# Kernel tuning notes

Hardware: AMD Instinct MI355X
Metric: run time of the kernel (lower is better)

The kernel has to match this reference:

```python
import jax, jax.numpy as jnp
import numpy as np

EMB = 384
HID = 256
HEADS = 4
HD = HID // HEADS  # 64
LAYERS = 2
M_DOCS = 32
TOTAL = 4096  # 1 query + 32 docs + 4063 sentences
LN_EPS = 1e-5


def _layernorm(x, scale, bias):
    mu = jnp.mean(x, axis=-1, keepdims=True)
    var = jnp.mean(jnp.square(x - mu), axis=-1, keepdims=True)
    return (x - mu) * jax.lax.rsqrt(var + LN_EPS) * scale + bias


def setup_inputs() -> dict:
    key = jax.random.key(0)
    ks = jax.random.split(key, 12)
    g = 0.05  # small init scale (stand-in for xavier)
    return {
        "node_embeddings": jax.random.normal(ks[0], (TOTAL, EMB), jnp.float32),
        "adj": jax.random.randint(ks[1], (TOTAL, TOTAL), 0, 2, jnp.int32),
        "num_docs": M_DOCS,
        "proj_w": jax.random.normal(ks[2], (HID, EMB), jnp.float32) * g,
        "proj_b": jnp.zeros((HID,), jnp.float32),
        "ln_scale": jnp.ones((LAYERS, HID), jnp.float32),
        "ln_bias": jnp.zeros((LAYERS, HID), jnp.float32),
        "gat_W": jax.random.normal(ks[3], (LAYERS, HEADS, HD, HID), jnp.float32) * g,
        "gat_a": jax.random.normal(ks[4], (LAYERS, HEADS, 2 * HD), jnp.float32) * g,
        "fusion_w": jax.random.normal(ks[5], (HID, 2 * HID + 2), jnp.float32) * g,
        "fusion_b": jnp.zeros((HID,), jnp.float32),
        "out_w": jax.random.normal(ks[6], (HID,), jnp.float32) * g,
        "out_b": jnp.float32(0.5),
    }


def reference(node_embeddings, adj, num_docs, proj_w, proj_b, ln_scale, ln_bias,
              gat_W, gat_a, fusion_w, fusion_b, out_w, out_b):
    T = node_embeddings.shape[0]
    M = num_docs
    N = T - 1 - M  # number of sentences
    # input projection + relu (dropout = identity in eval)
    h = jax.nn.relu(node_embeddings @ proj_w.T + proj_b)  # (T, HID)
    # query-guided sentence re-weighting
    q = h[0:1]                     # (1, HID)
    s = h[1 + M:]                  # (N, HID)
    qn = q / (jnp.linalg.norm(q, axis=1, keepdims=True) + 1e-8)
    sn = s / (jnp.linalg.norm(s, axis=1, keepdims=True) + 1e-8)
    cos = (qn @ sn.T).reshape(-1, 1)          # (N,1)
    s = s + 0.8 * q * cos
    h = jnp.concatenate([h[:1 + M], s], axis=0)
    mask = (adj == 0)[None]                   # (1,T,T)
    for i in range(LAYERS):
        res = h
        x = _layernorm(h, ln_scale[i], ln_bias[i])
        Wh = jnp.einsum('nd,hkd->hnk', x, gat_W[i])                # (H,T,HD)
        # concat-attention a.[Wh_i ; Wh_j] == a_src.Wh_i + a_dst.Wh_j
        src = jnp.einsum('hnk,hk->hn', Wh, gat_a[i, :, :HD])       # (H,T)
        dst = jnp.einsum('hnk,hk->hn', Wh, gat_a[i, :, HD:])       # (H,T)
        e = jax.nn.leaky_relu(src[:, :, None] + dst[:, None, :], 0.2)  # (H,T,T)
        e = jnp.where(mask, -jnp.inf, e)
        attn = jax.nn.softmax(e, axis=-1)                          # softmax over j
        hn = jnp.einsum('hij,hjk->hik', attn, Wh)                  # (H,T,HD)
        hcat = jnp.transpose(hn, (1, 0, 2)).reshape(T, HEADS * HD)
        h = 0.5 * jax.nn.relu(hcat) + 0.5 * res
    qh = h[0:1]
    sh = h[1 + M:]
    scores = (qh @ sh.T) / (HID ** 0.5)       # (1,N)
    aw = jax.nn.softmax(scores, axis=-1)
    awT = aw.T                                # (N,1)
    qw = qh * (awT + 0.5)                     # (N,HID)
    qnf = qh / (jnp.linalg.norm(qh, axis=1, keepdims=True) + 1e-8)
    snf = sh / (jnp.linalg.norm(sh, axis=1, keepdims=True) + 1e-8)
    cosf = (qnf @ snf.T).reshape(-1, 1)       # (N,1)
    feat = jnp.concatenate([sh, qw, cosf, awT], axis=1)  # (N, 2*HID+2)
    g = jax.nn.relu(feat @ fusion_w.T + fusion_b)
    out = g @ out_w + out_b                   # (N,)
    return out + 0.5 * cosf[:, 0]
```

## Files before the change

### kernel.cpp

```cpp
#include <hip/hip_runtime.h>
#include <hip/hip_bf16.h>
#include <stdint.h>

#define TOTAL 4096
#define EMB 384
#define MD 32
#define NDOCS (TOTAL - 1 - MD)
#define LN_EPS 1e-5f

typedef __hip_bfloat16 bf16;
typedef unsigned short ushort_t;
typedef __attribute__((ext_vector_type(8))) short short8;
typedef __attribute__((ext_vector_type(4))) float f32x4;
typedef __attribute__((ext_vector_type(2))) float f32x2;

__device__ __forceinline__ float ldf(const void* p, int i, int isbf) {
    return isbf ? __bfloat162float(((const bf16*)p)[i]) : ((const float*)p)[i];
}

__device__ __forceinline__ unsigned f2bf(float x) {
    return (__float_as_uint(x) + 0x8000u) >> 16;
}

__device__ __forceinline__ unsigned fenc(float f) {
    unsigned u = __float_as_uint(f);
    return (u >> 31) ? ~u : (u | 0x80000000u);
}
__device__ __forceinline__ float fdec(unsigned k) {
    return __uint_as_float((k & 0x80000000u) ? (k & 0x7FFFFFFFu) : ~k);
}

#define NTRANS ((EMB * 256 + 2 * 65536 + 514 * 256) / 256)
__global__ void k_adjmask(const int* adj, unsigned long long* maskb,
                          const uint16_t* embp, int* flag, unsigned* dmaxu,
                          const void* proj_w, const void* gat_W, const void* fusion_w,
                          float* projT, float* gatT, float* fwT) {
    __shared__ int red[4];
    int i = blockIdx.x, t = threadIdx.x;
    int w = t >> 6, l = t & 63;
    for (int c = w; c < 64; c += 4) {
        int a = adj[(size_t)i * TOTAL + c * 64 + l];
        unsigned long long m = __ballot(a != 0);
        if (l == 0) maskb[i * 64 + c] = m;
    }
    if (i == 0) {
        for (int idx = t; idx < 2048; idx += 256) dmaxu[idx] = 0x007FFFFFu;
    }
    if (i < NTRANS) {
        int cnt = 0;
        for (int k = t; k < 4096; k += 256) {
            uint16_t wd = embp[2 * k];
            int e = (wd >> 7) & 0xFF;
            if (e >= 100 && e <= 140) cnt++;
        }
        for (int o = 32; o > 0; o >>= 1) cnt += __shfl_down(cnt, o);
        if ((t & 63) == 0) red[t >> 6] = cnt;
        __syncthreads();
        int isbf = (red[0] + red[1] + red[2] + red[3] > 2048) ? 1 : 0;
        if (i == 0 && t == 0) flag[0] = isbf;
        int idx = i * 256 + t;
        if (idx < EMB * 256) {
            int d = idx >> 8, c = idx & 255;
            projT[idx] = ldf(proj_w, c * EMB + d, isbf);
        } else if (idx < EMB * 256 + 2 * 65536) {
            int r = idx - EMB * 256;
            int ll = r >> 16, rem = r & 65535;
            int d = rem >> 8, c = rem & 255;
            gatT[r] = ldf(gat_W, ll * 65536 + c * 256 + d, isbf);
        } else {
            int r = idx - (EMB * 256 + 2 * 65536);
            int j = r >> 8, c = r & 255;
            fwT[r] = ldf(fusion_w, c * 514 + j, isbf);
        }
    }
}

#define PR 8
__global__ void k_proj(const void* emb, const void* proj_b, const float* projT, float* h,
                       const int* flagp) {
    __shared__ float xs[PR][EMB];
    int isbf = flagp[0];
    int i0 = blockIdx.x * PR, t = threadIdx.x;
    for (int idx = t; idx < PR * EMB; idx += 256) {
        int r = idx / EMB, d = idx % EMB;
        xs[r][d] = ldf(emb, (i0 + r) * EMB + d, isbf);
    }
    __syncthreads();
    float acc[PR];
    float bias = ldf(proj_b, t, isbf);
#pragma unroll
    for (int r = 0; r < PR; r++) acc[r] = bias;
    for (int d0 = 0; d0 < EMB; d0 += 4) {
        float w0 = projT[d0 * 256 + t];
        float w1 = projT[(d0 + 1) * 256 + t];
        float w2 = projT[(d0 + 2) * 256 + t];
        float w3 = projT[(d0 + 3) * 256 + t];
#pragma unroll
        for (int r = 0; r < PR; r++) {
            float4 x = *(const float4*)&xs[r][d0];
            acc[r] = fmaf(x.x, w0, acc[r]);
            acc[r] = fmaf(x.y, w1, acc[r]);
            acc[r] = fmaf(x.z, w2, acc[r]);
            acc[r] = fmaf(x.w, w3, acc[r]);
        }
    }
#pragma unroll
    for (int r = 0; r < PR; r++) h[(size_t)(i0 + r) * 256 + t] = fmaxf(acc[r], 0.f);
}

__global__ __launch_bounds__(256) void k_cosupdate(float* h) {
    int t = threadIdx.x, W = t >> 6, lane = t & 63;
    float4* h4 = (float4*)h;
    float4 q4 = h4[lane];
    float a = q4.x * q4.x + q4.y * q4.y + q4.z * q4.z + q4.w * q4.w;
    for (int o = 32; o > 0; o >>= 1) a += __shfl_xor(a, o);
    float qn = sqrtf(a) + 1e-8f;
    int gw = blockIdx.x * 4 + W;
    for (int n = gw; n < NDOCS; n += 1024) {
        size_t ro = (size_t)(1 + MD + n) * 64;
        float4 s4 = h4[ro + lane];
        float b = s4.x * s4.x + s4.y * s4.y + s4.z * s4.z + s4.w * s4.w;
        float c = q4.x * s4.x + q4.y * s4.y + q4.z * s4.z + q4.w * s4.w;
        for (int o = 32; o > 0; o >>= 1) { b += __shfl_xor(b, o); c += __shfl_xor(c, o); }
        float k = 0.8f * (c / (qn * (sqrtf(b) + 1e-8f)));
        s4.x += k * q4.x; s4.y += k * q4.y; s4.z += k * q4.z; s4.w += k * q4.w;
        h4[ro + lane] = s4;
    }
}

#define LR 4
__global__ void k_ln_wh(float* h, const float* gatT, const void* ln_scale,
                        const void* ln_bias, const void* gat_a,
                        ushort_t* whswz, float* srcb, unsigned* d12g, unsigned* dmaxu,
                        const float* hnp, const float* lpart, int layer, int doepi,
                        const int* flagp) {
    __shared__ float xs[LR][256];
    __shared__ float red[2][LR][4];
    int isbf = flagp[0];
    int i0 = blockIdx.x * LR, t = threadIdx.x;
    int w = t >> 6, l = t & 63;
    float scale = ldf(ln_scale, layer * 256 + t, isbf);
    float bias = ldf(ln_bias, layer * 256 + t, isbf);
    float hv[LR];
    if (doepi) {
#pragma unroll
        for (int r = 0; r < LR; r++) {
            int i = i0 + r;
            float lsum = lpart[(size_t)w * 4096 + i] + lpart[(size_t)(4 + w) * 4096 + i] +
                         lpart[(size_t)(8 + w) * 4096 + i] + lpart[(size_t)(12 + w) * 4096 + i];
            float s = hnp[(size_t)i * 256 + t] + hnp[(size_t)TOTAL * 256 + i * 256 + t] +
                      hnp[(size_t)2 * TOTAL * 256 + i * 256 + t] +
                      hnp[(size_t)3 * TOTAL * 256 + i * 256 + t];
            float hn = 0.5f * fmaxf(s / lsum, 0.f) + 0.5f * h[(size_t)i * 256 + t];
            hv[r] = hn;
            h[(size_t)i * 256 + t] = hn;
        }
    } else {
#pragma unroll
        for (int r = 0; r < LR; r++) hv[r] = h[(size_t)(i0 + r) * 256 + t];
    }
#pragma unroll
    for (int r = 0; r < LR; r++) {
        float a = hv[r], b = hv[r] * hv[r];
        for (int o = 32; o > 0; o >>= 1) { a += __shfl_down(a, o); b += __shfl_down(b, o); }
        if (l == 0) { red[0][r][w] = a; red[1][r][w] = b; }
    }
    __syncthreads();
#pragma unroll
    for (int r = 0; r < LR; r++) {
        float mu = (red[0][r][0] + red[0][r][1] + red[0][r][2] + red[0][r][3]) * (1.f / 256.f);
        float var = (red[1][r][0] + red[1][r][1] + red[1][r][2] + red[1][r][3]) * (1.f / 256.f) - mu * mu;
        float x = (hv[r] - mu) * rsqrtf(var + LN_EPS) * scale + bias;
        xs[r][t] = x;
    }
    __syncthreads();
    const float* gT = gatT + layer * 65536;
    float acc[LR] = {0.f, 0.f, 0.f, 0.f};
    for (int d0 = 0; d0 < 256; d0 += 4) {
        float w0 = gT[d0 * 256 + t];
        float w1 = gT[(d0 + 1) * 256 + t];
        float w2 = gT[(d0 + 2) * 256 + t];
        float w3 = gT[(d0 + 3) * 256 + t];
#pragma unroll
        for (int r = 0; r < LR; r++) {
            float4 x = *(const float4*)&xs[r][d0];
            acc[r] = fmaf(x.x, w0, acc[r]);
            acc[r] = fmaf(x.y, w1, acc[r]);
            acc[r] = fmaf(x.z, w2, acc[r]);
            acc[r] = fmaf(x.w, w3, acc[r]);
        }
    }
    float av1 = ldf(gat_a, layer * 512 + w * 128 + l, isbf);
    float av2 = ldf(gat_a, layer * 512 + w * 128 + 64 + l, isbf);
    const float LOG2E = 1.44269504f;
    float mmax = -__builtin_inff();
#pragma unroll
    for (int r = 0; r < LR; r++) {
        int i = i0 + r;
        int off = (i >> 6) * 16384 + (t >> 6) * 4096 + ((i >> 3) & 7) * 512 +
                  ((t >> 4) & 3) * 128 + (t & 15) * 8 + (i & 7);
        whswz[off] = (ushort_t)f2bf(acc[r]);
        float sv = acc[r] * av1, dv = acc[r] * av2;
        for (int o = 32; o > 0; o >>= 1) { sv += __shfl_down(sv, o); dv += __shfl_down(dv, o); }
        if (l == 0) {
            srcb[w * 4096 + i] = sv;
            float D1 = exp2f(dv * LOG2E), D2 = exp2f(0.2f * dv * LOG2E);
            d12g[w * 4096 + i] = (f2bf(D2) << 16) | f2bf(D1);
            mmax = fmaxf(mmax, dv);
        }
    }
    if (l == 0) atomicMax(&dmaxu[(blockIdx.x & 63) * 16 + w], fenc(mmax));
}

#define TI 32
#define JS 4
__global__ __launch_bounds__(512) void k_pv(const ushort_t* whswz, const float* srcb,
                                            const unsigned* dmaxu, const unsigned* d12g,
                                            const unsigned long long* maskb,
                                            float* hnp, float* lpart) {
    __shared__ __align__(16) char smem[32768];
    __shared__ __align__(16) float lsh[4][2][4][4];
    __shared__ unsigned mlut[4];
    __shared__ float dmx[4];
    unsigned* d12s = (unsigned*)smem;
    unsigned long long* mbs = (unsigned long long*)(smem + 16384);
    float* srcs = (float*)(smem + 16384 + 4352);
    f32x4* accsh = (f32x4*)smem;
    int t = threadIdx.x;
    int W = t >> 6, lane = t & 63;
    int h = W & 3, kq = W >> 2;
    int quad = lane >> 4, c16 = lane & 15;
    int i0 = blockIdx.x * TI;
    int jbase = blockIdx.y * 1024;
    if (t < 4) mlut[t] = (t & 1 ? 0x0000FFFFu : 0u) | (t & 2 ? 0xFFFF0000u : 0u);
    if (t < 256) {
        int hh = t >> 6, sl = t & 63;
        float v = fdec(dmaxu[sl * 16 + hh]);
        for (int o = 32; o > 0; o >>= 1) v = fmaxf(v, __shfl_xor(v, o));
        if (sl == 0) dmx[hh] = v;
    }
    for (int idx = t; idx < TI * 16; idx += 512) {
        int r = idx >> 4, wd = idx & 15;
        mbs[r * 17 + wd] = maskb[(size_t)(i0 + r) * 64 + (jbase >> 6) + wd];
    }
    for (int idx = t; idx < 1024; idx += 512) {
        int hh = idx >> 8, j4 = idx & 255;
        ((uint4*)d12s)[idx] = ((const uint4*)(d12g + hh * 4096 + jbase))[j4];
    }
    if (t < 128) {
        int h2 = t >> 5, r = t & 31;
        srcs[h2 * 32 + r] = srcb[h2 * 4096 + i0 + r];
    }
    __syncthreads();
    const float LOG2E = 1.44269504f;
    float dm = dmx[h];
    float E1[2], E2[2];
#pragma unroll
    for (int rt = 0; rt < 2; rt++) {
        float src = srcs[h * 32 + rt * 16 + c16];
        float sd = src + dm;
        float rce = -fmaxf(sd, 0.2f * sd);
        E1[rt] = exp2f((src + rce) * LOG2E);
        E2[rt] = exp2f((0.2f * src + rce) * LOG2E);
    }
    f32x4 acc[2][4];
    f32x4 accl[2] = {(f32x4){0.f, 0.f, 0.f, 0.f}, (f32x4){0.f, 0.f, 0.f, 0.f}};
#pragma unroll
    for (int rt = 0; rt < 2; rt++)
#pragma unroll
        for (int ct = 0; ct < 4; ct++) acc[rt][ct] = (f32x4){0.f, 0.f, 0.f, 0.f};
    uint4 onesu;
    unsigned os = (c16 == 0) ? 0x3F803F80u : 0u;
    onesu.x = os; onesu.y = os; onesu.z = os; onesu.w = os;
    short8 bfones = __builtin_bit_cast(short8, onesu);
    const uint4* g4 = (const uint4*)whswz;
    size_t b0 = (size_t)(jbase >> 6) * 2048 + h * 512 + (kq * 4 + quad) * 64 + c16;
    uint4 bn[4];
#pragma unroll
    for (int ct = 0; ct < 4; ct++) bn[ct] = g4[b0 + ct * 16];
    for (int step = 0; step < 16; step++) {
        uint4 bc[4];
#pragma unroll
        for (int ct = 0; ct < 4; ct++) bc[ct] = bn[ct];
        if (step < 15) {
            size_t bs = b0 + (size_t)(step + 1) * 2048;
#pragma unroll
            for (int ct = 0; ct < 4; ct++) bn[ct] = g4[bs + ct * 16];
        }
        int jl0 = step * 64 + kq * 32 + quad * 8;
        unsigned mby[2];
#pragma unroll
        for (int rt = 0; rt < 2; rt++)
            mby[rt] = (unsigned)(mbs[(rt * 16 + c16) * 17 + step] >> (kq * 32 + quad * 8)) & 0xFFu;
        const uint4* dj = (const uint4*)&d12s[h * 1024 + jl0];
        uint4 da = dj[0], db = dj[1];
        unsigned dw[8] = {da.x, da.y, da.z, da.w, db.x, db.y, db.z, db.w};
        f32x2 D1[4], D2[4];
#pragma unroll
        for (int q = 0; q < 4; q++) {
            unsigned a = dw[2 * q], b = dw[2 * q + 1];
            D1[q] = (f32x2){__uint_as_float(a << 16), __uint_as_float(b << 16)};
            D2[q] = (f32x2){__uint_as_float(a & 0xFFFF0000u), __uint_as_float(b & 0xFFFF0000u)};
        }
        uint4 afu[2];
#pragma unroll
        for (int rt = 0; rt < 2; rt++) {
            unsigned pu[4];
#pragma unroll
            for (int q = 0; q < 4; q++) {
                f32x2 v1 = D1[q] * E1[rt];
                f32x2 v2 = D2[q] * E2[rt];
                f32x2 m = __builtin_elementwise_max(v1, v2);
                unsigned v = ((__float_as_uint(m.x) + 0x8000u) >> 16) |
                             ((__float_as_uint(m.y) + 0x8000u) & 0xFFFF0000u);
                pu[q] = v & mlut[(mby[rt] >> (2 * q)) & 3u];
            }
            afu[rt].x = pu[0]; afu[rt].y = pu[1]; afu[rt].z = pu[2]; afu[rt].w = pu[3];
        }
        short8 af0 = __builtin_bit_cast(short8, afu[0]);
        short8 af1 = __builtin_bit_cast(short8, afu[1]);
#pragma unroll
        for (int ct = 0; ct < 4; ct++) {
            short8 bf = __builtin_bit_cast(short8, bc[ct]);
            acc[0][ct] = __builtin_amdgcn_mfma_f32_16x16x32_bf16(af0, bf, acc[0][ct], 0, 0, 0);
            acc[1][ct] = __builtin_amdgcn_mfma_f32_16x16x32_bf16(af1, bf, acc[1][ct], 0, 0, 0);
        }
        accl[0] = __builtin_amdgcn_mfma_f32_16x16x32_bf16(af0, bfones, accl[0], 0, 0, 0);
        accl[1] = __builtin_amdgcn_mfma_f32_16x16x32_bf16(af1, bfones, accl[1], 0, 0, 0);
    }
    __syncthreads();
    if (kq == 1) {
#pragma unroll
        for (int rt = 0; rt < 2; rt++) {
#pragma unroll
            for (int ct = 0; ct < 4; ct++)
                accsh[((h * 2 + rt) * 4 + ct) * 64 + lane] = acc[rt][ct];
            if (c16 == 0) *(f32x4*)&lsh[h][rt][quad][0] = accl[rt];
        }
    }
    __syncthreads();
    if (kq == 0) {
        float* out = hnp + (size_t)blockIdx.y * (TOTAL * 256);
#pragma unroll
        for (int rt = 0; rt < 2; rt++) {
#pragma unroll
            for (int ct = 0; ct < 4; ct++) {
                f32x4 o = acc[rt][ct] + accsh[((h * 2 + rt) * 4 + ct) * 64 + lane];
#pragma unroll
                for (int rr = 0; rr < 4; rr++) {
                    int row = i0 + rt * 16 + quad * 4 + rr;
                    out[(size_t)row * 256 + h * 64 + ct * 16 + c16] = o[rr];
                }
            }
            if (c16 == 0) {
                f32x4 lv = accl[rt] + *(const f32x4*)&lsh[h][rt][quad][0];
#pragma unroll
                for (int rr = 0; rr < 4; rr++)
                    lpart[(size_t)(blockIdx.y * 4 + h) * 4096 + i0 + rt * 16 + quad * 4 + rr] = lv[rr];
            }
        }
    }
}

__global__ __launch_bounds__(256) void k_scores(float* h, const float* hnp, const float* lpart,
                                                float* qrow, float* scoresv, float* cosv) {
    int t = threadIdx.x, W = t >> 6, lane = t & 63;
    int hh = lane >> 4;
    float4* h4 = (float4*)h;
    const float4* p0 = (const float4*)hnp;
    const float4* p1 = p0 + (size_t)TOTAL * 64;
    const float4* p2 = p1 + (size_t)TOTAL * 64;
    const float4* p3 = p2 + (size_t)TOTAL * 64;
    int gw = blockIdx.x * 4 + W;
    float lq = lpart[(size_t)hh * 4096] + lpart[(size_t)(4 + hh) * 4096] +
               lpart[(size_t)(8 + hh) * 4096] + lpart[(size_t)(12 + hh) * 4096];
    float4 a0 = p0[lane], a1 = p1[lane], a2 = p2[lane], a3 = p3[lane];
    float4 hq = h4[lane];
    float invq = 1.f / lq;
    float4 q4;
    q4.x = 0.5f * fmaxf((a0.x + a1.x + a2.x + a3.x) * invq, 0.f) + 0.5f * hq.x;
    q4.y = 0.5f * fmaxf((a0.y + a1.y + a2.y + a3.y) * invq, 0.f) + 0.5f * hq.y;
    q4.z = 0.5f * fmaxf((a0.z + a1.z + a2.z + a3.z) * invq, 0.f) + 0.5f * hq.z;
    q4.w = 0.5f * fmaxf((a0.w + a1.w + a2.w + a3.w) * invq, 0.f) + 0.5f * hq.w;
    if (gw == 0) ((float4*)qrow)[lane] = q4;
    float a = q4.x * q4.x + q4.y * q4.y + q4.z * q4.z + q4.w * q4.w;
    for (int o = 32; o > 0; o >>= 1) a += __shfl_xor(a, o);
    float qn = sqrtf(a) + 1e-8f;
    for (int n = gw; n < NDOCS; n += 1024) {
        int row = 1 + MD + n;
        size_t ro = (size_t)row * 64;
        float ld = lpart[(size_t)hh * 4096 + row] + lpart[(size_t)(4 + hh) * 4096 + row] +
                   lpart[(size_t)(8 + hh) * 4096 + row] + lpart[(size_t)(12 + hh) * 4096 + row];
        float4 b0 = p0[ro + lane], b1 = p1[ro + lane], b2 = p2[ro + lane], b3 = p3[ro + lane];
        float4 ho = h4[ro + lane];
        float invd = 1.f / ld;
        float4 s4;
        s4.x = 0.5f * fmaxf((b0.x + b1.x + b2.x + b3.x) * invd, 0.f) + 0.5f * ho.x;
        s4.y = 0.5f * fmaxf((b0.y + b1.y + b2.y + b3.y) * invd, 0.f) + 0.5f * ho.y;
        s4.z = 0.5f * fmaxf((b0.z + b1.z + b2.z + b3.z) * invd, 0.f) + 0.5f * ho.z;
        s4.w = 0.5f * fmaxf((b0.w + b1.w + b2.w + b3.w) * invd, 0.f) + 0.5f * ho.w;
        h4[ro + lane] = s4;
        float b = s4.x * s4.x + s4.y * s4.y + s4.z * s4.z + s4.w * s4.w;
        float c = q4.x * s4.x + q4.y * s4.y + q4.z * s4.z + q4.w * s4.w;
        for (int o = 32; o > 0; o >>= 1) { b += __shfl_xor(b, o); c += __shfl_xor(c, o); }
        if (lane == 0) {
            scoresv[n] = c * (1.f / 16.f);
            cosv[n] = c / (qn * (sqrtf(b) + 1e-8f));
        }
    }
}

__global__ __launch_bounds__(1024) void k_softmax(const float* scoresv, float* awv) {
    __shared__ float red[16];
    int t = threadIdx.x;
    float m = -__builtin_inff();
    for (int n = t; n < NDOCS; n += 1024) m = fmaxf(m, scoresv[n]);
    for (int o = 32; o > 0; o >>= 1) m = fmaxf(m, __shfl_down(m, o));
    if ((t & 63) == 0) red[t >> 6] = m;
    __syncthreads();
    m = red[0];
#pragma unroll
    for (int i = 1; i < 16; i++) m = fmaxf(m, red[i]);
    __syncthreads();
    float s = 0.f;
    for (int n = t; n < NDOCS; n += 1024) s += __expf(scoresv[n] - m);
    for (int o = 32; o > 0; o >>= 1) s += __shfl_down(s, o);
    if ((t & 63) == 0) red[t >> 6] = s;
    __syncthreads();
    s = 0.f;
#pragma unroll
    for (int i = 0; i < 16; i++) s += red[i];
    float inv = 1.f / s;
    for (int n = t; n < NDOCS; n += 1024) awv[n] = __expf(scoresv[n] - m) * inv;
}

#define TN 8
__global__ __launch_bounds__(256) void k_fusion(const float* h, const float* qrow,
                                                const float* awv, const float* cosv,
                                                const float* fwT, const void* fusion_b,
                                                const void* out_w, const void* out_bp,
                                                void* outv, const int* flagp) {
    __shared__ float feats2[514][TN];
    __shared__ float qhs[256];
    __shared__ float red[TN][4];
    int isbf = flagp[0];
    int t = threadIdx.x;
    int n0 = blockIdx.x * TN;
    qhs[t] = qrow[t];
    __syncthreads();
    for (int idx = t; idx < 514 * TN; idx += 256) {
        int j = idx >> 3, r = idx & 7;
        int n = n0 + r;
        float v = 0.f;
        if (n < NDOCS) {
            if (j < 256) v = h[(size_t)(1 + MD + n) * 256 + j];
            else if (j < 512) v = qhs[j - 256] * (awv[n] + 0.5f);
            else if (j == 512) v = cosv[n];
            else v = awv[n];
        }
        feats2[j][r] = v;
    }
    __syncthreads();
    float acc[TN];
    float bk = ldf(fusion_b, t, isbf);
#pragma unroll
    for (int r = 0; r < TN; r++) acc[r] = bk;
    for (int j0 = 0; j0 < 512; j0 += 8) {
        float wv[8];
#pragma unroll
        for (int u = 0; u < 8; u++) wv[u] = fwT[(j0 + u) * 256 + t];
#pragma unroll
        for (int u = 0; u < 8; u++) {
            float4 fa = *(const float4*)&feats2[j0 + u][0];
            float4 fb = *(const float4*)&feats2[j0 + u][4];
            acc[0] = fmaf(fa.x, wv[u], acc[0]); acc[1] = fmaf(fa.y, wv[u], acc[1]);
            acc[2] = fmaf(fa.z, wv[u], acc[2]); acc[3] = fmaf(fa.w, wv[u], acc[3]);
            acc[4] = fmaf(fb.x, wv[u], acc[4]); acc[5] = fmaf(fb.y, wv[u], acc[5]);
            acc[6] = fmaf(fb.z, wv[u], acc[6]); acc[7] = fmaf(fb.w, wv[u], acc[7]);
        }
    }
#pragma unroll
    for (int j = 512; j < 514; j++) {
        float wv = fwT[j * 256 + t];
#pragma unroll
        for (int r = 0; r < TN; r++) acc[r] = fmaf(feats2[j][r], wv, acc[r]);
    }
    float ow = ldf(out_w, t, isbf);
    float outb = ldf(out_bp, 0, isbf);
#pragma unroll
    for (int r = 0; r < TN; r++) {
        float o = fmaxf(acc[r], 0.f) * ow;
        for (int off = 32; off > 0; off >>= 1) o += __shfl_down(o, off);
        if ((t & 63) == 0) red[r][t >> 6] = o;
    }
    __syncthreads();
    if (t < TN) {
        int n = n0 + t;
        if (n < NDOCS) {
            float o = red[t][0] + red[t][1] + red[t][2] + red[t][3] + outb + 0.5f * cosv[n];
            if (isbf) ((bf16*)outv)[n] = __float2bfloat16(o);
            else      ((float*)outv)[n] = o;
        }
    }
}

extern "C" void kernel_launch(void* const* d_in, const int* in_sizes, int n_in,
                              void* d_out, int out_size, void* d_ws, size_t ws_size,
                              hipStream_t stream) {
    const void* emb      = d_in[0];
    const int*  adj      = (const int*)d_in[1];
    const void* proj_w   = d_in[3];
    const void* proj_b   = d_in[4];
    const void* ln_scale = d_in[5];
    const void* ln_bias  = d_in[6];
    const void* gat_W    = d_in[7];
    const void* gat_a    = d_in[8];
    const void* fusion_w = d_in[9];
    const void* fusion_b = d_in[10];
    const void* out_w    = d_in[11];
    const void* out_b    = d_in[12];

    unsigned long long* maskb = (unsigned long long*)d_ws;
    int* flag = (int*)((char*)d_ws + (size_t)4096 * 64 * 8);
    float* f = (float*)((char*)d_ws + (size_t)4096 * 64 * 8 + 256);
    float* h       = f; f += 4096 * 256;
    float* srcb    = f; f += 4 * 4096;
    unsigned* d12g = (unsigned*)f; f += 4 * 4096;
    unsigned* dmaxu = (unsigned*)f; f += 2048;
    float* projT   = f; f += EMB * 256;
    float* gatT    = f; f += 2 * 65536;
    float* fwT     = f; f += 514 * 256;
    float* scoresv = f; f += 4096;
    float* cosv    = f; f += 4096;
    float* awv     = f; f += 4096;
    float* qrow    = f; f += 256;
    float* lpart   = f; f += 4 * 4 * 4096;
    ushort_t* whswz = (ushort_t*)f; f += 4096 * 256 / 2;
    float* hnp     = f; f += (size_t)JS * 4096 * 256;

    k_adjmask<<<dim3(4096), dim3(256), 0, stream>>>(adj, maskb, (const uint16_t*)emb, flag,
                                                    dmaxu, proj_w, gat_W, fusion_w,
                                                    projT, gatT, fwT);
    k_proj<<<dim3(TOTAL / PR), dim3(256), 0, stream>>>(emb, proj_b, projT, h, flag);
    k_cosupdate<<<dim3(256), dim3(256), 0, stream>>>(h);
    for (int layer = 0; layer < 2; layer++) {
        k_ln_wh<<<dim3(TOTAL / LR), dim3(256), 0, stream>>>(h, gatT, ln_scale, ln_bias, gat_a,
                                                            whswz, srcb, d12g, dmaxu + layer * 1024,
                                                            hnp, lpart, layer, layer, flag);
        k_pv<<<dim3(TOTAL / TI, JS), dim3(512), 0, stream>>>(whswz, srcb, dmaxu + layer * 1024,
                                                             d12g, maskb, hnp, lpart);
    }
    k_scores<<<dim3(256), dim3(256), 0, stream>>>(h, hnp, lpart, qrow, scoresv, cosv);
    k_softmax<<<dim3(1), dim3(1024), 0, stream>>>(scoresv, awv);
    k_fusion<<<dim3((NDOCS + TN - 1) / TN), dim3(256), 0, stream>>>(h, qrow, awv, cosv,
                                                                    fwT, fusion_b, out_w,
                                                                    out_b, (void*)d_out, flag);
}
```

Baseline: 308.7 us.

## Fuse cosine update into LN kernel and softmax into scores/fusion kernels

Removes the standalone cosine-update kernel and folds the query-guided sentence update into the first layer's LayerNorm/Wh kernel, whose block size is raised to 8 rows. Removes the single-block softmax kernel: the scores kernel now emits per-wave online max/sum partials, and every fusion block recombines those 1024 partials to compute its own attention weights. This cuts two launches and a serialized one-block reduction, at the cost of redundant partial reduction in each fusion block and extra syncs in the LN kernel.

```diff
diff --git a/kernel.cpp b/kernel.cpp
--- a/kernel.cpp
+++ b/kernel.cpp
@@ -108,27 +108,7 @@
     for (int r = 0; r < PR; r++) h[(size_t)(i0 + r) * 256 + t] = fmaxf(acc[r], 0.f);
 }
 
-__global__ __launch_bounds__(256) void k_cosupdate(float* h) {
-    int t = threadIdx.x, W = t >> 6, lane = t & 63;
-    float4* h4 = (float4*)h;
-    float4 q4 = h4[lane];
-    float a = q4.x * q4.x + q4.y * q4.y + q4.z * q4.z + q4.w * q4.w;
-    for (int o = 32; o > 0; o >>= 1) a += __shfl_xor(a, o);
-    float qn = sqrtf(a) + 1e-8f;
-    int gw = blockIdx.x * 4 + W;
-    for (int n = gw; n < NDOCS; n += 1024) {
-        size_t ro = (size_t)(1 + MD + n) * 64;
-        float4 s4 = h4[ro + lane];
-        float b = s4.x * s4.x + s4.y * s4.y + s4.z * s4.z + s4.w * s4.w;
-        float c = q4.x * s4.x + q4.y * s4.y + q4.z * s4.z + q4.w * s4.w;
-        for (int o = 32; o > 0; o >>= 1) { b += __shfl_xor(b, o); c += __shfl_xor(c, o); }
-        float k = 0.8f * (c / (qn * (sqrtf(b) + 1e-8f)));
-        s4.x += k * q4.x; s4.y += k * q4.y; s4.z += k * q4.z; s4.w += k * q4.w;
-        h4[ro + lane] = s4;
-    }
-}
-
-#define LR 4
+#define LR 8
 __global__ void k_ln_wh(float* h, const float* gatT, const void* ln_scale,
                         const void* ln_bias, const void* gat_a,
                         ushort_t* whswz, float* srcb, unsigned* d12g, unsigned* dmaxu,
@@ -136,6 +116,8 @@
                         const int* flagp) {
     __shared__ float xs[LR][256];
     __shared__ float red[2][LR][4];
+    __shared__ float qsm[256];
+    __shared__ float qred[4];
     int isbf = flagp[0];
     int i0 = blockIdx.x * LR, t = threadIdx.x;
     int w = t >> 6, l = t & 63;
@@ -156,8 +138,38 @@
             h[(size_t)i * 256 + t] = hn;
         }
     } else {
+        qsm[t] = h[t];
 #pragma unroll
         for (int r = 0; r < LR; r++) hv[r] = h[(size_t)(i0 + r) * 256 + t];
+        __syncthreads();
+        float qv = qsm[t];
+        {
+            float a = qv * qv;
+            for (int o = 32; o > 0; o >>= 1) a += __shfl_down(a, o);
+            if (l == 0) qred[w] = a;
+        }
+#pragma unroll
+        for (int r = 0; r < LR; r++) {
+            float b = hv[r] * hv[r], c = qv * hv[r];
+            for (int o = 32; o > 0; o >>= 1) { b += __shfl_down(b, o); c += __shfl_down(c, o); }
+            if (l == 0) { red[0][r][w] = b; red[1][r][w] = c; }
+        }
+        __syncthreads();
+        if (i0 + LR > 1 + MD) {
+            float qn = sqrtf(qred[0] + qred[1] + qred[2] + qred[3]) + 1e-8f;
+#pragma unroll
+            for (int r = 0; r < LR; r++) {
+                int i = i0 + r;
+                if (i >= 1 + MD) {
+                    float bs = red[0][r][0] + red[0][r][1] + red[0][r][2] + red[0][r][3];
+                    float cs = red[1][r][0] + red[1][r][1] + red[1][r][2] + red[1][r][3];
+                    float k = 0.8f * (cs / (qn * (sqrtf(bs) + 1e-8f)));
+                    hv[r] += k * qv;
+                    h[(size_t)i * 256 + t] = hv[r];
+                }
+            }
+        }
+        __syncthreads();
     }
 #pragma unroll
     for (int r = 0; r < LR; r++) {
@@ -175,7 +187,9 @@
     }
     __syncthreads();
     const float* gT = gatT + layer * 65536;
-    float acc[LR] = {0.f, 0.f, 0.f, 0.f};
+    float acc[LR];
+#pragma unroll
+    for (int r = 0; r < LR; r++) acc[r] = 0.f;
     for (int d0 = 0; d0 < 256; d0 += 4) {
         float w0 = gT[d0 * 256 + t];
         float w1 = gT[(d0 + 1) * 256 + t];
@@ -363,7 +377,8 @@
 }
 
 __global__ __launch_bounds__(256) void k_scores(float* h, const float* hnp, const float* lpart,
-                                                float* qrow, float* scoresv, float* cosv) {
+                                                float* qrow, float* scoresv, float* cosv,
+                                                float* swp) {
     int t = threadIdx.x, W = t >> 6, lane = t & 63;
     int hh = lane >> 4;
     float4* h4 = (float4*)h;
@@ -386,6 +401,7 @@
     float a = q4.x * q4.x + q4.y * q4.y + q4.z * q4.z + q4.w * q4.w;
     for (int o = 32; o > 0; o >>= 1) a += __shfl_xor(a, o);
     float qn = sqrtf(a) + 1e-8f;
+    float mw = -__builtin_inff(), sw = 0.f;
     for (int n = gw; n < NDOCS; n += 1024) {
         int row = 1 + MD + n;
         size_t ro = (size_t)row * 64;
@@ -403,50 +419,57 @@
         float b = s4.x * s4.x + s4.y * s4.y + s4.z * s4.z + s4.w * s4.w;
         float c = q4.x * s4.x + q4.y * s4.y + q4.z * s4.z + q4.w * s4.w;
         for (int o = 32; o > 0; o >>= 1) { b += __shfl_xor(b, o); c += __shfl_xor(c, o); }
+        float sc = c * (1.f / 16.f);
         if (lane == 0) {
-            scoresv[n] = c * (1.f / 16.f);
+            scoresv[n] = sc;
             cosv[n] = c / (qn * (sqrtf(b) + 1e-8f));
         }
-    }
-}
-
-__global__ __launch_bounds__(1024) void k_softmax(const float* scoresv, float* awv) {
-    __shared__ float red[16];
-    int t = threadIdx.x;
-    float m = -__builtin_inff();
-    for (int n = t; n < NDOCS; n += 1024) m = fmaxf(m, scoresv[n]);
-    for (int o = 32; o > 0; o >>= 1) m = fmaxf(m, __shfl_down(m, o));
-    if ((t & 63) == 0) red[t >> 6] = m;
-    __syncthreads();
-    m = red[0];
-#pragma unroll
-    for (int i = 1; i < 16; i++) m = fmaxf(m, red[i]);
-    __syncthreads();
-    float s = 0.f;
-    for (int n = t; n < NDOCS; n += 1024) s += __expf(scoresv[n] - m);
-    for (int o = 32; o > 0; o >>= 1) s += __shfl_down(s, o);
-    if ((t & 63) == 0) red[t >> 6] = s;
-    __syncthreads();
-    s = 0.f;
-#pragma unroll
-    for (int i = 0; i < 16; i++) s += red[i];
-    float inv = 1.f / s;
-    for (int n = t; n < NDOCS; n += 1024) awv[n] = __expf(scoresv[n] - m) * inv;
+        float mn = fmaxf(mw, sc);
+        sw = sw * __expf(mw - mn) + __expf(sc - mn);
+        mw = mn;
+    }
+    if (lane == 0) { swp[2 * gw] = mw; swp[2 * gw + 1] = sw; }
 }
 
 #define TN 8
 __global__ __launch_bounds__(256) void k_fusion(const float* h, const float* qrow,
-                                                const float* awv, const float* cosv,
+                                                const float* scoresv, const float* swp,
+                                                const float* cosv,
                                                 const float* fwT, const void* fusion_b,
                                                 const void* out_w, const void* out_bp,
                                                 void* outv, const int* flagp) {
     __shared__ float feats2[514][TN];
     __shared__ float qhs[256];
     __shared__ float red[TN][4];
+    __shared__ float reds[2][4];
+    __shared__ float aws[TN];
     int isbf = flagp[0];
     int t = threadIdx.x;
     int n0 = blockIdx.x * TN;
     qhs[t] = qrow[t];
+    float M = -__builtin_inff(), S = 0.f;
+    for (int idx = t; idx < 1024; idx += 256) {
+        float pm = swp[2 * idx], ps = swp[2 * idx + 1];
+        float mn = fmaxf(M, pm);
+        S = S * __expf(M - mn) + ps * __expf(pm - mn);
+        M = mn;
+    }
+    for (int o = 32; o > 0; o >>= 1) {
+        float m2 = __shfl_xor(M, o), s2 = __shfl_xor(S, o);
+        float mn = fmaxf(M, m2);
+        S = S * __expf(M - mn) + s2 * __expf(m2 - mn);
+        M = mn;
+    }
+    if ((t & 63) == 0) { reds[0][t >> 6] = M; reds[1][t >> 6] = S; }
+    __syncthreads();
+    float Mf = fmaxf(fmaxf(reds[0][0], reds[0][1]), fmaxf(reds[0][2], reds[0][3]));
+    float Sf = reds[1][0] * __expf(reds[0][0] - Mf) + reds[1][1] * __expf(reds[0][1] - Mf) +
+               reds[1][2] * __expf(reds[0][2] - Mf) + reds[1][3] * __expf(reds[0][3] - Mf);
+    float invS = 1.f / Sf;
+    if (t < TN) {
+        int n = n0 + t;
+        aws[t] = (n < NDOCS) ? __expf(scoresv[n] - Mf) * invS : 0.f;
+    }
     __syncthreads();
     for (int idx = t; idx < 514 * TN; idx += 256) {
         int j = idx >> 3, r = idx & 7;
@@ -454,9 +477,9 @@
         float v = 0.f;
         if (n < NDOCS) {
             if (j < 256) v = h[(size_t)(1 + MD + n) * 256 + j];
-            else if (j < 512) v = qhs[j - 256] * (awv[n] + 0.5f);
+            else if (j < 512) v = qhs[j - 256] * (aws[r] + 0.5f);
             else if (j == 512) v = cosv[n];
-            else v = awv[n];
+            else v = aws[r];
         }
         feats2[j][r] = v;
     }
@@ -532,7 +555,7 @@
     float* fwT     = f; f += 514 * 256;
     float* scoresv = f; f += 4096;
     float* cosv    = f; f += 4096;
-    float* awv     = f; f += 4096;
+    float* swpart  = f; f += 4096;
     float* qrow    = f; f += 256;
     float* lpart   = f; f += 4 * 4 * 4096;
     ushort_t* whswz = (ushort_t*)f; f += 4096 * 256 / 2;
@@ -542,7 +565,6 @@
                                                     dmaxu, proj_w, gat_W, fusion_w,
                                                     projT, gatT, fwT);
     k_proj<<<dim3(TOTAL / PR), dim3(256), 0, stream>>>(emb, proj_b, projT, h, flag);
-    k_cosupdate<<<dim3(256), dim3(256), 0, stream>>>(h);
     for (int layer = 0; layer < 2; layer++) {
         k_ln_wh<<<dim3(TOTAL / LR), dim3(256), 0, stream>>>(h, gatT, ln_scale, ln_bias, gat_a,
                                                             whswz, srcb, d12g, dmaxu + layer * 1024,
@@ -550,9 +572,8 @@
         k_pv<<<dim3(TOTAL / TI, JS), dim3(512), 0, stream>>>(whswz, srcb, dmaxu + layer * 1024,
                                                              d12g, maskb, hnp, lpart);
     }
-    k_scores<<<dim3(256), dim3(256), 0, stream>>>(h, hnp, lpart, qrow, scoresv, cosv);
-    k_softmax<<<dim3(1), dim3(1024), 0, stream>>>(scoresv, awv);
-    k_fusion<<<dim3((NDOCS + TN - 1) / TN), dim3(256), 0, stream>>>(h, qrow, awv, cosv,
-                                                                    fwT, fusion_b, out_w,
+    k_scores<<<dim3(256), dim3(256), 0, stream>>>(h, hnp, lpart, qrow, scoresv, cosv, swpart);
+    k_fusion<<<dim3((NDOCS + TN - 1) / TN), dim3(256), 0, stream>>>(h, qrow, scoresv, swpart,
+                                                                    cosv, fwT, fusion_b, out_w,
                                                                     out_b, (void*)d_out, flag);
 }
```

New measurement: 304.1 us. About the same (-1.5%).
